# Kernel optimization log

Measured on AMD Instinct MI355X. Metric: run time of the kernel, lower is better.

## Reference

```python
import jax, jax.numpy as jnp
import numpy as np

RATIO = 4   # compression ratio (group size)
H = 6       # index heads
D = 64      # index head dim = max(8, 768//6//2)
TOPK = 8    # index_topk
EPS = 1e-6  # rms_norm eps


def rms_norm(x):
    return x * jax.lax.rsqrt(jnp.mean(jnp.square(x), axis=-1, keepdims=True) + EPS)


def setup_inputs() -> dict:
    key = jax.random.key(0)
    k1, k2, k3, k4, k5 = jax.random.split(key, 5)
    B, T, E = 4, 4096, 768
    s = 0.02
    return {
        "x": jax.random.normal(k1, (B, T, E), jnp.float32),
        "wq": jax.random.normal(k2, (E, H * D), jnp.float32) * s,
        "wk": jax.random.normal(k3, (E, H * D), jnp.float32) * s,
        "wg": jax.random.normal(k4, (E, H * D), jnp.float32) * s,
        "ape": jax.random.normal(k5, (RATIO, H, D), jnp.float32) * s,
    }


def reference(x, wq, wk, wg, ape):
    B, T, E = x.shape
    G = -(-T // RATIO)          # ceil(T / ratio)
    pad = G * RATIO - T

    # --- compress keys: gated pooling over ratio-groups ---
    k = (x @ wk).reshape(B, T, H, D)
    gate = (x @ wg).reshape(B, T, H, D)
    if pad:
        k = jnp.pad(k, ((0, 0), (0, pad), (0, 0), (0, 0)))
        gate = jnp.pad(gate, ((0, 0), (0, pad), (0, 0), (0, 0)), constant_values=-jnp.inf)
    k = k.reshape(B, G, RATIO, H, D)
    gate = gate.reshape(B, G, RATIO, H, D) + ape[None, None]
    w = jax.nn.softmax(gate.astype(jnp.float32), axis=2).astype(k.dtype)
    keys = rms_norm(jnp.sum(k * w, axis=2))           # [B,G,H,D]
    group_ends = jnp.minimum(jnp.arange(RATIO - 1, G * RATIO, RATIO), T - 1)  # [G]

    # --- query-key scores ---
    q = rms_norm((x @ wq).reshape(B, T, H, D))
    scores = jnp.einsum('bthd,bghd->bhtg', q, keys) * (D ** -0.5)
    scores = jnp.mean(scores, axis=1)                 # [B,T,G]

    # --- causal mask over group ends, then top-k selection ---
    causal = group_ends[None, None, :] <= jnp.arange(T)[None, :, None]  # [1,T,G]
    scores = jnp.where(causal, scores, -jnp.inf)
    topk = min(TOPK, G)
    _, sel = jax.lax.top_k(scores, topk)              # [B,T,topk]

    # scatter selected indices into boolean mask
    bi = jnp.arange(B)[:, None, None]
    ti = jnp.arange(T)[None, :, None]
    mask = jnp.zeros((B, T, G), dtype=bool).at[bi, ti, sel].set(True)
    return (mask & causal, group_ends)
```

## Files before the change

kernel.cpp:

```cpp
#include <hip/hip_runtime.h>
#include <hip/hip_bf16.h>
#include <math.h>

#define B_    4
#define T_    4096
#define E_    768
#define H_    6
#define D_    64
#define HD_   384
#define G_    1024
#define RATIO_ 4
#define TOPK_ 8
#define MT_   (B_*T_)
#define NS_   1152

typedef __attribute__((ext_vector_type(8))) short short8;
typedef __attribute__((ext_vector_type(4))) float f32x4;
typedef __hip_bfloat16 bf16;

#define GLD16(g, l) __builtin_amdgcn_global_load_lds( \
    (const __attribute__((address_space(1))) void*)(g), \
    (__attribute__((address_space(3))) void*)(l), 16, 0, 0)

static __device__ __forceinline__ unsigned short f2bf(float f) {
  bf16 h = __float2bfloat16(f);
  return __builtin_bit_cast(unsigned short, h);
}
static __device__ __forceinline__ unsigned umax_(unsigned a, unsigned b) { return a > b ? a : b; }
static __device__ __forceinline__ unsigned umin_(unsigned a, unsigned b) { return a > b ? b : a; }

__global__ __launch_bounds__(256) void cvt_x_kernel(
    const float* __restrict__ in, bf16* __restrict__ out)
{
  size_t i = (size_t)blockIdx.x * 256 + threadIdx.x;
  const float4* p = reinterpret_cast<const float4*>(in) + i * 2;
  float4 v0 = p[0], v1 = p[1];
  float f[8] = {v0.x, v0.y, v0.z, v0.w, v1.x, v1.y, v1.z, v1.w};
  union { unsigned short u[8]; short8 v; } r;
#pragma unroll
  for (int k = 0; k < 8; ++k) r.u[k] = f2bf(f[k]);
  *reinterpret_cast<short8*>(out + i * 8) = r.v;
}

__global__ __launch_bounds__(256) void cvt_w_t(
    const float* __restrict__ wq, const float* __restrict__ wk,
    const float* __restrict__ wg, bf16* __restrict__ outbase)
{
  const int z = blockIdx.z;
  const float* src = z == 0 ? wq : (z == 1 ? wk : wg);
  __shared__ float t[32][33];
  int r = threadIdx.x >> 5, c = threadIdx.x & 31;
  int k0 = blockIdx.x * 32, n0 = blockIdx.y * 32;
#pragma unroll
  for (int i = 0; i < 4; ++i)
    t[r + i * 8][c] = src[(size_t)(k0 + r + i * 8) * HD_ + n0 + c];
  __syncthreads();
#pragma unroll
  for (int i = 0; i < 4; ++i) {
    int cc = n0 + r + i * 8;
    int ro = (z == 0) ? cc : 384 + ((cc >> 4) << 5) + ((z - 1) << 4) + (cc & 15);
    outbase[(size_t)ro * E_ + k0 + c] = __float2bfloat16(t[c][r + i * 8]);
  }
}

__global__ __launch_bounds__(256, 3) void gemm_qkg_mfma(
    const bf16* __restrict__ X, const bf16* __restrict__ Ws,
    const float* __restrict__ ape, bf16* __restrict__ Q,
    bf16* __restrict__ keys)
{
  __shared__ bf16 lds[2][8192];
  const int tid = threadIdx.x;
  const int lane = tid & 63, wv = tid >> 6;
  const int ll = lane & 15, lh = lane >> 4;
  const int m0 = blockIdx.x * 128, n0 = blockIdx.y * 128;
  const int srow = tid >> 3;
  const int sslot = (((tid & 7) ^ ((tid >> 3) & 7)) << 3);
  const bf16* pS = Ws + (size_t)(n0 + srow) * E_ + sslot;
  const bf16* pA0 = X + (size_t)(m0 + wv * 32 + ll) * E_ + lh * 8;
  const bf16* pA1 = pA0 + (size_t)16 * E_;

#define STAGE(b, k0) do { \
    char* base_ = (char*)&lds[b][0] + tid * 16; \
    GLD16(pS + (k0),            base_); \
    GLD16(pS + 32 * E_ + (k0),  base_ + 4096); \
    GLD16(pS + 64 * E_ + (k0),  base_ + 8192); \
    GLD16(pS + 96 * E_ + (k0),  base_ + 12288); \
  } while (0)
#define LOAD_A(dst, k0) do { \
    dst[0][0] = *reinterpret_cast<const short8*>(pA0 + (k0)); \
    dst[0][1] = *reinterpret_cast<const short8*>(pA0 + (k0) + 32); \
    dst[1][0] = *reinterpret_cast<const short8*>(pA1 + (k0)); \
    dst[1][1] = *reinterpret_cast<const short8*>(pA1 + (k0) + 32); \
  } while (0)

  f32x4 acc[2][8];
#pragma unroll
  for (int m = 0; m < 2; ++m)
#pragma unroll
    for (int n = 0; n < 8; ++n) acc[m][n] = (f32x4){0.f, 0.f, 0.f, 0.f};

  short8 curA[2][2], nxtA[2][2];
  LOAD_A(curA, 0);
  STAGE(0, 0);
#pragma unroll
  for (int m = 0; m < 2; ++m)
#pragma unroll
    for (int s = 0; s < 2; ++s) nxtA[m][s] = curA[m][s];

#pragma unroll
  for (int k = 0; k < 12; ++k) {
    const int k0 = k * 64;
    if (k < 11) {
      LOAD_A(nxtA, k0 + 64);
      STAGE((k + 1) & 1, k0 + 64);
    }
    if (k < 11) asm volatile("s_waitcnt vmcnt(8)" ::: "memory");
    else        asm volatile("s_waitcnt vmcnt(0)" ::: "memory");
    __builtin_amdgcn_s_barrier();
    __builtin_amdgcn_sched_barrier(0);
    const bf16* Lb = &lds[k & 1][0];
    short8 b0[8];
#pragma unroll
    for (int n = 0; n < 8; ++n)
      b0[n] = *reinterpret_cast<const short8*>(
          &Lb[(n * 16 + ll) * 64 + ((lh ^ (ll & 7)) << 3)]);
    asm volatile("s_waitcnt lgkmcnt(0)" ::: "memory");
    __builtin_amdgcn_sched_barrier(0);
#pragma unroll
    for (int m = 0; m < 2; ++m)
#pragma unroll
      for (int n = 0; n < 8; ++n)
        acc[m][n] = __builtin_amdgcn_mfma_f32_16x16x32_bf16(curA[m][0], b0[n], acc[m][n], 0, 0, 0);
    short8 b1[8];
#pragma unroll
    for (int n = 0; n < 8; ++n)
      b1[n] = *reinterpret_cast<const short8*>(
          &Lb[(n * 16 + ll) * 64 + (((4 + lh) ^ (ll & 7)) << 3)]);
    asm volatile("s_waitcnt lgkmcnt(0)" ::: "memory");
    __builtin_amdgcn_sched_barrier(0);
    __builtin_amdgcn_s_barrier();
#pragma unroll
    for (int m = 0; m < 2; ++m)
#pragma unroll
      for (int n = 0; n < 8; ++n)
        acc[m][n] = __builtin_amdgcn_mfma_f32_16x16x32_bf16(curA[m][1], b1[n], acc[m][n], 0, 0, 0);
#pragma unroll
    for (int m = 0; m < 2; ++m)
#pragma unroll
      for (int s = 0; s < 2; ++s) curA[m][s] = nxtA[m][s];
  }
#undef STAGE
#undef LOAD_A

  if (blockIdx.y < 3) {
#pragma unroll
    for (int m = 0; m < 2; ++m)
#pragma unroll
      for (int j = 0; j < 4; ++j) {
        int row = m0 + wv * 32 + m * 16 + lh * 4 + j;
#pragma unroll
        for (int h = 0; h < 2; ++h) {
          float ss = 0.f;
#pragma unroll
          for (int n = 4 * h; n < 4 * h + 4; ++n) ss += acc[m][n][j] * acc[m][n][j];
          ss += __shfl_xor(ss, 1, 64); ss += __shfl_xor(ss, 2, 64);
          ss += __shfl_xor(ss, 4, 64); ss += __shfl_xor(ss, 8, 64);
          float scl = rsqrtf(ss * (1.0f / D_) + 1e-6f);
#pragma unroll
          for (int n = 4 * h; n < 4 * h + 4; ++n)
            Q[(size_t)row * HD_ + n0 + n * 16 + ll] =
                __float2bfloat16(acc[m][n][j] * scl);
        }
      }
  } else {
    const int hcb = (n0 - 384) >> 1;
    float apev[4][4];
#pragma unroll
    for (int p = 0; p < 4; ++p) {
      int hc = hcb + p * 16 + ll;
#pragma unroll
      for (int j = 0; j < 4; ++j) apev[p][j] = ape[j * HD_ + hc];
    }
#pragma unroll
    for (int m = 0; m < 2; ++m) {
      float pooled[4];
#pragma unroll
      for (int p = 0; p < 4; ++p) {
        float g0 = acc[m][2 * p + 1][0] + apev[p][0];
        float g1 = acc[m][2 * p + 1][1] + apev[p][1];
        float g2 = acc[m][2 * p + 1][2] + apev[p][2];
        float g3 = acc[m][2 * p + 1][3] + apev[p][3];
        float mx = fmaxf(fmaxf(g0, g1), fmaxf(g2, g3));
        float e0 = expf(g0 - mx), e1 = expf(g1 - mx);
        float e2 = expf(g2 - mx), e3 = expf(g3 - mx);
        float inv = 1.0f / (e0 + e1 + e2 + e3);
        pooled[p] = (acc[m][2 * p][0] * e0 + acc[m][2 * p][1] * e1 +
                     acc[m][2 * p][2] * e2 + acc[m][2 * p][3] * e3) * inv;
      }
      float ss = pooled[0] * pooled[0] + pooled[1] * pooled[1] +
                 pooled[2] * pooled[2] + pooled[3] * pooled[3];
      ss += __shfl_xor(ss, 1, 64); ss += __shfl_xor(ss, 2, 64);
      ss += __shfl_xor(ss, 4, 64); ss += __shfl_xor(ss, 8, 64);
      float scl = rsqrtf(ss * (1.0f / D_) + 1e-6f);
      int prow = (m0 >> 2) + wv * 8 + m * 4 + lh;
#pragma unroll
      for (int p = 0; p < 4; ++p)
        keys[(size_t)prow * HD_ + hcb + p * 16 + ll] =
            __float2bfloat16(pooled[p] * scl);
    }
  }
}

#define CEx(a, bb) { unsigned h_ = umax_(a, bb), l_ = umin_(a, bb); a = h_; bb = l_; }
#define MERGE4() \
  _Pragma("unroll") \
  for (int st = 0; st < 2; ++st) { \
    const int off = 16 << st; \
    unsigned p0 = (unsigned)__shfl_xor((int)v0, off, 64); \
    unsigned p1 = (unsigned)__shfl_xor((int)v1, off, 64); \
    unsigned p2 = (unsigned)__shfl_xor((int)v2, off, 64); \
    unsigned p3 = (unsigned)__shfl_xor((int)v3, off, 64); \
    unsigned p4 = (unsigned)__shfl_xor((int)v4, off, 64); \
    unsigned p5 = (unsigned)__shfl_xor((int)v5, off, 64); \
    unsigned p6 = (unsigned)__shfl_xor((int)v6, off, 64); \
    unsigned p7 = (unsigned)__shfl_xor((int)v7, off, 64); \
    unsigned w0 = umax_(v0, p7), w1 = umax_(v1, p6); \
    unsigned w2 = umax_(v2, p5), w3 = umax_(v3, p4); \
    unsigned w4 = umax_(v4, p3), w5 = umax_(v5, p2); \
    unsigned w6 = umax_(v6, p1), w7 = umax_(v7, p0); \
    CEx(w0, w4); CEx(w1, w5); CEx(w2, w6); CEx(w3, w7); \
    CEx(w0, w2); CEx(w1, w3); CEx(w4, w6); CEx(w5, w7); \
    CEx(w0, w1); CEx(w2, w3); CEx(w4, w5); CEx(w6, w7); \
    v0 = w0; v1 = w1; v2 = w2; v3 = w3; v4 = w4; v5 = w5; v6 = w6; v7 = w7; \
  }

__global__ __launch_bounds__(128, 2) void score_topk8(
    const bf16* __restrict__ Qall, const bf16* __restrict__ Kall,
    unsigned* __restrict__ fin)
{
  __shared__ bf16 kbuf[2][12288];
  const int x = blockIdx.x;
  const int b = blockIdx.y;
  const int s = (b < 2) ? x : 127 - x;
  const int R0 = s << 5;
  const int tid = threadIdx.x;
  const int w = tid >> 6;
  const int lane = tid & 63;
  const int ll = lane & 15, lh = lane >> 4;

  const bf16* Qb = Qall + (size_t)b * T_ * HD_;
  const bf16* Kb = Kall + (size_t)b * G_ * HD_;
  const int t = R0 + 16 * w + ll;
  const int gmax = (t + 1) >> 2;
  const int ntw = ((((R0 + 16 * w) >> 2) + 4) + 31) >> 5;
  const int nt  = ((((R0 + 16) >> 2) + 4) + 31) >> 5;

  const bf16* ksrc[12];
  int sdst[12];
#pragma unroll
  for (int i = 0; i < 12; ++i) {
    int u = (12 * w + i) * 64 + lane;
    int r = u / 48, sp = u - r * 48;
    int sl = sp ^ (r & 7);
    ksrc[i] = Kb + (size_t)r * HD_ + sl * 8;
    sdst[i] = u * 16;
  }
  short8 qf[12];
  {
    const bf16* pQ = Qb + (size_t)t * HD_ + lh * 8;
#pragma unroll
    for (int k = 0; k < 12; ++k)
      qf[k] = *reinterpret_cast<const short8*>(pQ + k * 32);
  }

#define KSTAGE(bf, g0) do { \
    char* bb_ = (char*)&kbuf[bf][0]; \
    _Pragma("unroll") \
    for (int i = 0; i < 12; ++i) \
      GLD16(ksrc[i] + (size_t)(g0) * HD_, bb_ + sdst[i]); \
  } while (0)

  unsigned v0 = 0, v1 = 0, v2 = 0, v3 = 0, v4 = 0, v5 = 0, v6 = 0, v7 = 0;
#define INS(xx) do { unsigned k_ = (xx), t_; \
    t_ = umax_(v0, k_); k_ = umin_(v0, k_); v0 = t_; \
    t_ = umax_(v1, k_); k_ = umin_(v1, k_); v1 = t_; \
    t_ = umax_(v2, k_); k_ = umin_(v2, k_); v2 = t_; \
    t_ = umax_(v3, k_); k_ = umin_(v3, k_); v3 = t_; \
    t_ = umax_(v4, k_); k_ = umin_(v4, k_); v4 = t_; \
    t_ = umax_(v5, k_); k_ = umin_(v5, k_); v5 = t_; \
    t_ = umax_(v6, k_); k_ = umin_(v6, k_); v6 = t_; \
    t_ = umax_(v7, k_); k_ = umin_(v7, k_); v7 = t_; } while (0)

  KSTAGE(0, 0);
  for (int mg = 0; mg < nt; ++mg) {
    if (mg + 1 < nt) {
      KSTAGE((mg + 1) & 1, (mg + 1) * 32);
      asm volatile("s_waitcnt vmcnt(12)" ::: "memory");
    } else {
      asm volatile("s_waitcnt vmcnt(0)" ::: "memory");
    }
    __builtin_amdgcn_s_barrier();
    __builtin_amdgcn_sched_barrier(0);
    if (mg < ntw) {
      const char* Lb = (const char*)&kbuf[mg & 1][0];
      f32x4 acc0 = (f32x4){0.f, 0.f, 0.f, 0.f};
      f32x4 acc1 = (f32x4){0.f, 0.f, 0.f, 0.f};
#pragma unroll
      for (int kk = 0; kk < 12; ++kk) {
        int sl = 4 * kk + lh;
        short8 k0 = *reinterpret_cast<const short8*>(
            Lb + (size_t)ll * 768 + ((sl ^ (ll & 7)) << 4));
        short8 k1 = *reinterpret_cast<const short8*>(
            Lb + (size_t)(16 + ll) * 768 + ((sl ^ (ll & 7)) << 4));
        acc0 = __builtin_amdgcn_mfma_f32_16x16x32_bf16(k0, qf[kk], acc0, 0, 0, 0);
        acc1 = __builtin_amdgcn_mfma_f32_16x16x32_bf16(k1, qf[kk], acc1, 0, 0, 0);
      }
      const int g0 = mg * 32;
#pragma unroll
      for (int j = 0; j < 4; ++j) {
        int g = g0 + lh * 4 + j;
        float xv = acc0[j] + 512.0f;
        unsigned key = (g < gmax)
            ? ((__builtin_bit_cast(unsigned, xv) & 0xFFFFFC00u) |
               (unsigned)(1023 - g))
            : 0u;
        INS(key);
      }
#pragma unroll
      for (int j = 0; j < 4; ++j) {
        int g = g0 + 16 + lh * 4 + j;
        float xv = acc1[j] + 512.0f;
        unsigned key = (g < gmax)
            ? ((__builtin_bit_cast(unsigned, xv) & 0xFFFFFC00u) |
               (unsigned)(1023 - g))
            : 0u;
        INS(key);
      }
    }
    __builtin_amdgcn_s_barrier();
  }
#undef INS
#undef KSTAGE

  MERGE4();

  if (lh == 0) {
    unsigned* pp = fin + ((size_t)b * T_ + R0 + 16 * w + ll) * 8;
    reinterpret_cast<int4*>(pp)[0] = make_int4((int)v0, (int)v1, (int)v2, (int)v3);
    reinterpret_cast<int4*>(pp)[1] = make_int4((int)v4, (int)v5, (int)v6, (int)v7);
  }
}

__global__ __launch_bounds__(256) void mask_write(
    const unsigned* __restrict__ fin, int* __restrict__ mask,
    int* __restrict__ ends)
{
  const int tid = threadIdx.x;
  if (blockIdx.x == 0) {
    int g = tid;
#pragma unroll
    for (int c = 0; c < 4; ++c, g += 256) {
      int e = (g << 2) + 3;
      ends[g] = e < T_ - 1 ? e : T_ - 1;
    }
  }
  const size_t RB = (size_t)blockIdx.x * 64;
  int4* m4 = reinterpret_cast<int4*>(mask + RB * G_);
  const int4 z = make_int4(0, 0, 0, 0);
#pragma unroll
  for (int r = 0; r < 64; ++r) m4[r * 256 + tid] = z;
  asm volatile("s_waitcnt vmcnt(0)" ::: "memory");
  __syncthreads();
  if (tid < 64) {
    const unsigned* pp = fin + (RB + tid) * 8;
    int4 q0 = reinterpret_cast<const int4*>(pp)[0];
    int4 q1 = reinterpret_cast<const int4*>(pp)[1];
    int* rb = mask + (RB + tid) * G_;
    if (q0.x) rb[1023 - ((unsigned)q0.x & 1023)] = 1;
    if (q0.y) rb[1023 - ((unsigned)q0.y & 1023)] = 1;
    if (q0.z) rb[1023 - ((unsigned)q0.z & 1023)] = 1;
    if (q0.w) rb[1023 - ((unsigned)q0.w & 1023)] = 1;
    if (q1.x) rb[1023 - ((unsigned)q1.x & 1023)] = 1;
    if (q1.y) rb[1023 - ((unsigned)q1.y & 1023)] = 1;
    if (q1.z) rb[1023 - ((unsigned)q1.z & 1023)] = 1;
    if (q1.w) rb[1023 - ((unsigned)q1.w & 1023)] = 1;
  }
}

extern "C" void kernel_launch(void* const* d_in, const int* in_sizes, int n_in,
                              void* d_out, int out_size, void* d_ws, size_t ws_size,
                              hipStream_t stream)
{
  const float* x   = (const float*)d_in[0];
  const float* wq  = (const float*)d_in[1];
  const float* wk  = (const float*)d_in[2];
  const float* wg  = (const float*)d_in[3];
  const float* ape = (const float*)d_in[4];

  bf16* Ws   = (bf16*)d_ws;
  bf16* qb   = Ws + (size_t)NS_ * E_;
  bf16* keys = qb + (size_t)MT_ * HD_;
  unsigned* fin = (unsigned*)(keys + (size_t)B_ * G_ * HD_);

  bf16* xb = (bf16*)d_out;

  cvt_x_kernel<<<dim3(MT_ * E_ / 8 / 256), dim3(256), 0, stream>>>(x, xb);
  cvt_w_t<<<dim3(E_ / 32, HD_ / 32, 3), dim3(256), 0, stream>>>(wq, wk, wg, Ws);

  gemm_qkg_mfma<<<dim3(MT_ / 128, NS_ / 128), dim3(256), 0, stream>>>(
      xb, Ws, ape, qb, keys);

  score_topk8<<<dim3(128, B_), dim3(128), 0, stream>>>(qb, keys, fin);

  mask_write<<<dim3(256), dim3(256), 0, stream>>>(
      fin, (int*)d_out, (int*)d_out + (size_t)B_ * T_ * G_);
}
```

Before: 108.3 us.

## Fuse mask zeroing and top-k scatter into score kernel

Removes the separate mask_write kernel and its intermediate top-k buffer. Each score block now zeroes its 32-row slice of the output mask at the start, so those stores overlap with the scoring and top-k work. After the merge it scatters the selected indices straight from registers, and one block writes group_ends. This saves a kernel launch and the write and reread of the intermediate buffer. The cost is heavy store traffic sharing bandwidth with the score kernel's K loads, and correctness now relies on the __syncthreads ordering the zero stores before the scattered ones.

```diff
diff --git a/kernel.cpp b/kernel.cpp
--- a/kernel.cpp
+++ b/kernel.cpp
@@ -236,7 +236,7 @@
 
 __global__ __launch_bounds__(128, 2) void score_topk8(
     const bf16* __restrict__ Qall, const bf16* __restrict__ Kall,
-    unsigned* __restrict__ fin)
+    int* __restrict__ mask, int* __restrict__ ends)
 {
   __shared__ bf16 kbuf[2][12288];
   const int x = blockIdx.x;
@@ -248,6 +248,23 @@
   const int lane = tid & 63;
   const int ll = lane & 15, lh = lane >> 4;
 
+  if (x == 0 && b == 0) {
+    int g = tid;
+#pragma unroll
+    for (int c = 0; c < 8; ++c, g += 128) {
+      int e = (g << 2) + 3;
+      ends[g] = e < T_ - 1 ? e : T_ - 1;
+    }
+  }
+
+  int* mbase = mask + ((size_t)b * T_ + R0) * G_;
+  {
+    int4* m4 = reinterpret_cast<int4*>(mbase);
+    const int4 z = make_int4(0, 0, 0, 0);
+#pragma unroll
+    for (int i = 0; i < 64; ++i) m4[i * 128 + tid] = z;
+  }
+
   const bf16* Qb = Qall + (size_t)b * T_ * HD_;
   const bf16* Kb = Kall + (size_t)b * G_ * HD_;
   const int t = R0 + 16 * w + ll;
@@ -344,46 +361,17 @@
 
   MERGE4();
 
+  __syncthreads();
   if (lh == 0) {
-    unsigned* pp = fin + ((size_t)b * T_ + R0 + 16 * w + ll) * 8;
-    reinterpret_cast<int4*>(pp)[0] = make_int4((int)v0, (int)v1, (int)v2, (int)v3);
-    reinterpret_cast<int4*>(pp)[1] = make_int4((int)v4, (int)v5, (int)v6, (int)v7);
-  }
-}
-
-__global__ __launch_bounds__(256) void mask_write(
-    const unsigned* __restrict__ fin, int* __restrict__ mask,
-    int* __restrict__ ends)
-{
-  const int tid = threadIdx.x;
-  if (blockIdx.x == 0) {
-    int g = tid;
-#pragma unroll
-    for (int c = 0; c < 4; ++c, g += 256) {
-      int e = (g << 2) + 3;
-      ends[g] = e < T_ - 1 ? e : T_ - 1;
-    }
-  }
-  const size_t RB = (size_t)blockIdx.x * 64;
-  int4* m4 = reinterpret_cast<int4*>(mask + RB * G_);
-  const int4 z = make_int4(0, 0, 0, 0);
-#pragma unroll
-  for (int r = 0; r < 64; ++r) m4[r * 256 + tid] = z;
-  asm volatile("s_waitcnt vmcnt(0)" ::: "memory");
-  __syncthreads();
-  if (tid < 64) {
-    const unsigned* pp = fin + (RB + tid) * 8;
-    int4 q0 = reinterpret_cast<const int4*>(pp)[0];
-    int4 q1 = reinterpret_cast<const int4*>(pp)[1];
-    int* rb = mask + (RB + tid) * G_;
-    if (q0.x) rb[1023 - ((unsigned)q0.x & 1023)] = 1;
-    if (q0.y) rb[1023 - ((unsigned)q0.y & 1023)] = 1;
-    if (q0.z) rb[1023 - ((unsigned)q0.z & 1023)] = 1;
-    if (q0.w) rb[1023 - ((unsigned)q0.w & 1023)] = 1;
-    if (q1.x) rb[1023 - ((unsigned)q1.x & 1023)] = 1;
-    if (q1.y) rb[1023 - ((unsigned)q1.y & 1023)] = 1;
-    if (q1.z) rb[1023 - ((unsigned)q1.z & 1023)] = 1;
-    if (q1.w) rb[1023 - ((unsigned)q1.w & 1023)] = 1;
+    int* rb = mbase + (size_t)(16 * w + ll) * G_;
+    if (v0) rb[1023 - (v0 & 1023)] = 1;
+    if (v1) rb[1023 - (v1 & 1023)] = 1;
+    if (v2) rb[1023 - (v2 & 1023)] = 1;
+    if (v3) rb[1023 - (v3 & 1023)] = 1;
+    if (v4) rb[1023 - (v4 & 1023)] = 1;
+    if (v5) rb[1023 - (v5 & 1023)] = 1;
+    if (v6) rb[1023 - (v6 & 1023)] = 1;
+    if (v7) rb[1023 - (v7 & 1023)] = 1;
   }
 }
 
@@ -400,7 +388,6 @@
   bf16* Ws   = (bf16*)d_ws;
   bf16* qb   = Ws + (size_t)NS_ * E_;
   bf16* keys = qb + (size_t)MT_ * HD_;
-  unsigned* fin = (unsigned*)(keys + (size_t)B_ * G_ * HD_);
 
   bf16* xb = (bf16*)d_out;
 
@@ -410,8 +397,6 @@
   gemm_qkg_mfma<<<dim3(MT_ / 128, NS_ / 128), dim3(256), 0, stream>>>(
       xb, Ws, ape, qb, keys);
 
-  score_topk8<<<dim3(128, B_), dim3(128), 0, stream>>>(qb, keys, fin);
-
-  mask_write<<<dim3(256), dim3(256), 0, stream>>>(
-      fin, (int*)d_out, (int*)d_out + (size_t)B_ * T_ * G_);
-}
+  score_topk8<<<dim3(128, B_), dim3(128), 0, stream>>>(
+      qb, keys, (int*)d_out, (int*)d_out + (size_t)B_ * T_ * G_);
+}
```

Result: faster. 105.7 us (-2.4%).
